# Optimization experiments

Hardware: AMD Instinct MI355X
Metric: run time of the kernel (lower is better)

Reference implementation:

```python
import jax, jax.numpy as jnp
import numpy as np

T, E, H, K, WCNT, L = 131072, 512, 512, 1024, 50000, 128
NUM_LAYERS = 1


def setup_inputs() -> dict:
    key = jax.random.key(0)
    ks = jax.random.split(key, 12)
    f32 = jnp.float32
    return {
        "topic": jax.random.randint(ks[0], (L,), 0, WCNT, dtype=jnp.int32),
        "score_s": jax.random.uniform(ks[1], (1,), dtype=f32),
        "emb": jax.random.normal(ks[2], (WCNT, E), dtype=f32) * 0.05,
        "h": jax.random.normal(ks[3], (NUM_LAYERS, 1, H), dtype=f32) * 0.05,
        "vs": jax.random.normal(ks[4], (T, E), dtype=f32) * 0.05,
        "hs": jax.random.normal(ks[5], (T, 1, H), dtype=f32) * 0.05,
        "w_ih": jax.random.normal(ks[6], (3 * H, 2 * E + 1), dtype=f32) * 0.02,
        "w_hh": jax.random.normal(ks[7], (3 * H, H), dtype=f32) * 0.02,
        "b_ih": jnp.zeros((3 * H,), f32),
        "b_hh": jnp.zeros((3 * H,), f32),
        "w_score": jax.random.normal(ks[8], (1, E + 2 * H + 1), dtype=f32) * 0.02,
        "b_score": jnp.zeros((1,), f32),
    }


def _forward(topic, score_s, emb, h, vs, hs, w_ih, w_hh, b_ih, b_hh, w_score, b_score):
    # topic embedding: mean of word vectors -> v [E]
    v = emb[topic].mean(axis=0)
    # dot-product attention over growing history
    alpha = vs @ v                               # [T]
    vals, idx = jax.lax.top_k(alpha, K)          # top-k similar past items
    a = jax.nn.softmax(vals)                     # [K]
    hs_flat = hs.reshape(-1, NUM_LAYERS * H)     # [T, H]
    attn_h = a @ hs_flat[idx]                    # [H] weighted combine of gathered states
    length = jnp.full((1,), K, dtype=v.dtype)
    # with_last=True: cat([v, attn_h, h, length])
    pred_v = jnp.concatenate([v, attn_h, h.reshape(-1), length])[None, :]  # [1, E+2H+1]
    score = pred_v @ w_score.T + b_score         # [1, 1]
    # score_mode='double': split v by correctness of s
    pos = (score_s >= 0.5).astype(v.dtype)[0]
    x = jnp.concatenate([v * pos, v * (1.0 - pos), score_s])  # [2E+1]
    # single GRU step (torch gate layout: r, z, n)
    h_prev = h.reshape(H)
    gi = w_ih @ x + b_ih
    gh = w_hh @ h_prev + b_hh
    r = jax.nn.sigmoid(gi[:H] + gh[:H])
    z = jax.nn.sigmoid(gi[H:2 * H] + gh[H:2 * H])
    n = jnp.tanh(gi[2 * H:] + r * gh[2 * H:])
    h_new = ((1.0 - z) * n + z * h_prev).reshape(NUM_LAYERS, 1, H)
    # LSTMA updates the history
    vs_new = jnp.concatenate([vs, v[None, :]], axis=0)
    hs_new = jnp.concatenate([hs, h_new], axis=0)
    return score, h_new, vs_new, hs_new


def reference(topic, score_s, emb, h, vs, hs, w_ih, w_hh, b_ih, b_hh, w_score, b_score):
    return _forward(topic, score_s, emb, h, vs, hs, w_ih, w_hh, b_ih, b_hh, w_score, b_score)
```

## Files before the change

kernel.cpp:

```cpp
#include <hip/hip_runtime.h>
#include <math.h>

constexpr int T_ = 131072;
constexpr int E_ = 512;
constexpr int H_ = 512;
constexpr int K_ = 1024;
constexpr int L_ = 128;

typedef __attribute__((ext_vector_type(4))) float f32x4;

constexpr size_t OFF_V     = 0;
constexpr size_t OFF_ALPHA = 512;
constexpr size_t OFF_HIST1 = OFF_ALPHA + T_;
constexpr size_t OFF_HIST2 = OFF_HIST1 + 65536;
constexpr size_t OFF_CNT   = OFF_HIST2 + 65536;
constexpr size_t OFF_INFO  = OFF_CNT + 2;
constexpr size_t OFF_VALS  = OFF_INFO + 8;
constexpr size_t OFF_IDX   = OFF_VALS + K_;
constexpr size_t OFF_GI    = OFF_IDX + K_;
constexpr size_t OFF_GH    = OFF_GI + 3 * H_;

constexpr int ZERO_N = 65536 + 65536 + 2;

constexpr size_t OUT_VS = 513;
constexpr size_t OUT_HS = 513 + (size_t)(T_ + 1) * E_;

__device__ __forceinline__ unsigned fkey(float f) {
    unsigned u = __float_as_uint(f);
    return (u & 0x80000000u) ? ~u : (u | 0x80000000u);
}

__global__ __launch_bounds__(1024) void k_init(const int* __restrict__ topic,
                                               const float* __restrict__ emb,
                                               float* __restrict__ ws_v,
                                               unsigned* __restrict__ zero_base,
                                               float* __restrict__ out) {
    if (blockIdx.x == gridDim.x - 1) {
        __shared__ float part[512];
        int t = threadIdx.x;
        int e = t & 511, g = t >> 9;
        float s = 0.f;
        #pragma unroll 8
        for (int l = g * 64; l < g * 64 + 64; ++l) {
            int tp = topic[l];
            s += emb[(size_t)tp * E_ + e];
        }
        if (g == 1) part[e] = s;
        __syncthreads();
        if (g == 0) {
            float v = (s + part[e]) * (1.0f / L_);
            ws_v[e] = v;
            out[OUT_VS + (size_t)T_ * E_ + e] = v;
        }
    } else {
        int i = blockIdx.x * blockDim.x + threadIdx.x;
        if (i < ZERO_N) zero_base[i] = 0u;
    }
}

__global__ __launch_bounds__(256) void k_mega(const float* __restrict__ vs,
                                              const float* __restrict__ hs,
                                              const float* __restrict__ ws_v,
                                              float* __restrict__ alpha,
                                              unsigned* __restrict__ hist1,
                                              float* __restrict__ out) {
    int wave = threadIdx.x >> 6, lane = threadIdx.x & 63;
    int b = blockIdx.x;
    bool is_vs = b < (T_ / 4);
    int row = (is_vs ? b : b - T_ / 4) * 4 + wave;
    const f32x4* src4 = (const f32x4*)((is_vs ? vs : hs) + (size_t)row * E_);
    f32x4 a0 = __builtin_nontemporal_load(&src4[lane]);
    f32x4 a1 = __builtin_nontemporal_load(&src4[lane + 64]);
    if (is_vs) {
        const f32x4* v4 = (const f32x4*)ws_v;
        f32x4 b0 = v4[lane];
        f32x4 b1 = v4[lane + 64];
        float dot = 0.f;
        dot = fmaf(a0.x, b0.x, dot); dot = fmaf(a0.y, b0.y, dot);
        dot = fmaf(a0.z, b0.z, dot); dot = fmaf(a0.w, b0.w, dot);
        dot = fmaf(a1.x, b1.x, dot); dot = fmaf(a1.y, b1.y, dot);
        dot = fmaf(a1.z, b1.z, dot); dot = fmaf(a1.w, b1.w, dot);
        #pragma unroll
        for (int m = 32; m; m >>= 1) dot += __shfl_xor(dot, m, 64);
        if (lane == 0) {
            alpha[row] = dot;
            atomicAdd(&hist1[fkey(dot) >> 16], 1u);
        }
    }
    int nl = (lane + 1) & 63;
    float n0x = __shfl(a0.x, nl, 64), n0y = __shfl(a0.y, nl, 64), n0z = __shfl(a0.z, nl, 64);
    float n1x = __shfl(a1.x, nl, 64), n1y = __shfl(a1.y, nl, 64), n1z = __shfl(a1.z, nl, 64);
    float* dst = out + (is_vs ? OUT_VS : OUT_HS) + (size_t)row * E_;
    f32x4* d4 = (f32x4*)(dst + 3);
    bool last = (lane == 63);
    f32x4 lo;
    lo.x = a0.w;
    lo.y = last ? n1x : n0x;
    lo.z = last ? n1y : n0y;
    lo.w = last ? n1z : n0z;
    __builtin_nontemporal_store(lo, &d4[lane]);
    if (!last) {
        f32x4 hi;
        hi.x = a1.w; hi.y = n1x; hi.z = n1y; hi.w = n1z;
        __builtin_nontemporal_store(hi, &d4[lane + 64]);
    }
    if (lane == 0) { dst[0] = a0.x; dst[1] = a0.y; dst[2] = a0.z; }
    if (last) dst[511] = a1.w;
}

__global__ __launch_bounds__(256) void k_scan(const unsigned* __restrict__ hist,
                                              unsigned* __restrict__ info, int pass) {
    __shared__ unsigned ps[256];
    __shared__ unsigned s_chunk, s_above;
    int t = threadIdx.x;
    unsigned Kwant = (pass == 0) ? (unsigned)K_ : ((unsigned)K_ - info[1]);
    unsigned base = 65536u - (unsigned)(t + 1) * 256u;
    unsigned s = 0;
    for (int j = 0; j < 256; ++j) s += hist[base + j];
    ps[t] = s;
    __syncthreads();
    #pragma unroll
    for (int off = 1; off < 256; off <<= 1) {
        unsigned v = (t >= off) ? ps[t - off] : 0u;
        __syncthreads();
        ps[t] += v;
        __syncthreads();
    }
    unsigned incl = ps[t], excl = incl - s;
    if (excl < Kwant && incl >= Kwant) { s_chunk = (unsigned)t; s_above = excl; }
    __syncthreads();
    unsigned c = s_chunk;
    unsigned Kw2 = Kwant - s_above;
    unsigned bin = 65535u - c * 256u - (unsigned)t;
    unsigned b = hist[bin];
    __syncthreads();
    ps[t] = b;
    __syncthreads();
    #pragma unroll
    for (int off = 1; off < 256; off <<= 1) {
        unsigned v = (t >= off) ? ps[t - off] : 0u;
        __syncthreads();
        ps[t] += v;
        __syncthreads();
    }
    unsigned inc2 = ps[t], ex2 = inc2 - b;
    if (ex2 < Kw2 && inc2 >= Kw2) {
        unsigned cnt_above = s_above + ex2;
        if (pass == 0) { info[0] = bin; info[1] = cnt_above; }
        else {
            info[2] = (info[0] << 16) | bin;
            info[3] = info[1] + cnt_above;
            info[4] = (unsigned)K_ - info[3];
        }
    }
}

__global__ __launch_bounds__(256) void k_hist2(const float* __restrict__ alpha,
                                               const unsigned* __restrict__ info,
                                               unsigned* __restrict__ hist2) {
    int i = blockIdx.x * blockDim.x + threadIdx.x;
    unsigned key = fkey(alpha[i]);
    if ((key >> 16) == info[0]) atomicAdd(&hist2[key & 0xFFFFu], 1u);
}

__global__ __launch_bounds__(256) void k_select(const float* __restrict__ alpha,
                                                const unsigned* __restrict__ info,
                                                unsigned* __restrict__ cnt,
                                                float* __restrict__ vals,
                                                int* __restrict__ idx) {
    int i = blockIdx.x * blockDim.x + threadIdx.x;
    float a = alpha[i];
    unsigned key = fkey(a);
    unsigned thr = info[2];
    if (key > thr) {
        unsigned p = atomicAdd(&cnt[0], 1u);
        vals[p] = a; idx[p] = i;
    } else if (key == thr) {
        unsigned t = atomicAdd(&cnt[1], 1u);
        if (t < info[4]) {
            unsigned p = info[3] + t;
            vals[p] = a; idx[p] = i;
        }
    }
}

__global__ __launch_bounds__(512) void k_attn(const float* __restrict__ hs,
                                              const float* __restrict__ vals,
                                              const int* __restrict__ idx,
                                              float* __restrict__ part) {
    __shared__ float red[512];
    int t = threadIdx.x, j = blockIdx.x;
    float v0 = vals[t], v1 = vals[t + 512];
    red[t] = fmaxf(v0, v1);
    __syncthreads();
    for (int s = 256; s > 0; s >>= 1) { if (t < s) red[t] = fmaxf(red[t], red[t + s]); __syncthreads(); }
    float m = red[0];
    __syncthreads();
    red[t] = expf(v0 - m) + expf(v1 - m);
    __syncthreads();
    for (int s = 256; s > 0; s >>= 1) { if (t < s) red[t] += red[t + s]; __syncthreads(); }
    float S = red[0];
    float acc = 0.f;
    #pragma unroll
    for (int k = j * 8; k < j * 8 + 8; ++k) {
        float w = expf(vals[k] - m) / S;
        acc = fmaf(w, hs[(size_t)idx[k] * E_ + t], acc);
    }
    part[(size_t)j * E_ + t] = acc;
}

__global__ __launch_bounds__(256) void k_gru(const float* __restrict__ wih,
                                             const float* __restrict__ whh,
                                             const float* __restrict__ bih,
                                             const float* __restrict__ bhh,
                                             const float* __restrict__ ws_v,
                                             const float* __restrict__ score_s,
                                             const float* __restrict__ h_in,
                                             float* __restrict__ gi,
                                             float* __restrict__ gh) {
    __shared__ float x[1025 + 512];
    int t = threadIdx.x;
    float ss = score_s[0];
    float pos = ss >= 0.5f ? 1.f : 0.f;
    for (int c = t; c < 1025; c += 256) {
        float xv;
        if (c < 512)       xv = ws_v[c] * pos;
        else if (c < 1024) xv = ws_v[c - 512] * (1.f - pos);
        else               xv = ss;
        x[c] = xv;
    }
    for (int c = t; c < 512; c += 256) x[1025 + c] = h_in[c];
    __syncthreads();
    int wave = t >> 6, lane = t & 63;
    int row = blockIdx.x * 4 + wave;
    const float* wr = wih + (size_t)row * 1025;
    float s1 = 0.f;
    for (int c = lane; c < 1025; c += 64) s1 = fmaf(wr[c], x[c], s1);
    const float* hr = whh + (size_t)row * 512;
    float s2 = 0.f;
    #pragma unroll
    for (int c = lane; c < 512; c += 64) s2 = fmaf(hr[c], x[1025 + c], s2);
    #pragma unroll
    for (int m = 32; m; m >>= 1) {
        s1 += __shfl_xor(s1, m, 64);
        s2 += __shfl_xor(s2, m, 64);
    }
    if (lane == 0) { gi[row] = s1 + bih[row]; gh[row] = s2 + bhh[row]; }
}

__global__ __launch_bounds__(512) void k_final(const float* __restrict__ gi,
                                               const float* __restrict__ gh,
                                               const float* __restrict__ h_in,
                                               const float* __restrict__ part,
                                               const float* __restrict__ ws_v,
                                               const float* __restrict__ w_score,
                                               const float* __restrict__ b_score,
                                               float* __restrict__ out) {
    __shared__ float red[512];
    int j = threadIdx.x;
    float r = 1.f / (1.f + expf(-(gi[j] + gh[j])));
    float z = 1.f / (1.f + expf(-(gi[H_ + j] + gh[H_ + j])));
    float n = tanhf(gi[2 * H_ + j] + r * gh[2 * H_ + j]);
    float hp = h_in[j];
    float hn = (1.f - z) * n + z * hp;
    out[1 + j] = hn;
    out[OUT_HS + (size_t)T_ * E_ + j] = hn;
    float attn = 0.f;
    for (int jj = 0; jj < 128; ++jj) attn += part[(size_t)jj * E_ + j];
    float d = ws_v[j] * w_score[j] + attn * w_score[512 + j] + hp * w_score[1024 + j];
    if (j == 0) d += 1024.0f * w_score[1536] + b_score[0];
    red[j] = d;
    __syncthreads();
    for (int s = 256; s > 0; s >>= 1) { if (j < s) red[j] += red[j + s]; __syncthreads(); }
    if (j == 0) out[0] = red[0];
}

extern "C" void kernel_launch(void* const* d_in, const int* in_sizes, int n_in,
                              void* d_out, int out_size, void* d_ws, size_t ws_size,
                              hipStream_t stream) {
    const int*   topic   = (const int*)d_in[0];
    const float* score_s = (const float*)d_in[1];
    const float* emb     = (const float*)d_in[2];
    const float* h_in    = (const float*)d_in[3];
    const float* vs      = (const float*)d_in[4];
    const float* hs      = (const float*)d_in[5];
    const float* w_ih    = (const float*)d_in[6];
    const float* w_hh    = (const float*)d_in[7];
    const float* b_ih    = (const float*)d_in[8];
    const float* b_hh    = (const float*)d_in[9];
    const float* w_score = (const float*)d_in[10];
    const float* b_score = (const float*)d_in[11];
    float* out = (float*)d_out;

    float*    wsf   = (float*)d_ws;
    float*    v_ws  = wsf + OFF_V;
    float*    alpha = wsf + OFF_ALPHA;
    unsigned* hist1 = (unsigned*)(wsf + OFF_HIST1);
    unsigned* hist2 = (unsigned*)(wsf + OFF_HIST2);
    unsigned* cnt   = (unsigned*)(wsf + OFF_CNT);
    unsigned* info  = (unsigned*)(wsf + OFF_INFO);
    float*    vals  = wsf + OFF_VALS;
    int*      idx   = (int*)(wsf + OFF_IDX);
    float*    part  = wsf + OFF_ALPHA;
    float*    gi    = wsf + OFF_GI;
    float*    gh    = wsf + OFF_GH;

    hipLaunchKernelGGL(k_init, dim3(130), dim3(1024), 0, stream,
                       topic, emb, v_ws, hist1, out);
    hipLaunchKernelGGL(k_mega, dim3(2 * (T_ / 4)), dim3(256), 0, stream,
                       vs, hs, v_ws, alpha, hist1, out);
    hipLaunchKernelGGL(k_scan, dim3(1), dim3(256), 0, stream, hist1, info, 0);
    hipLaunchKernelGGL(k_hist2, dim3(T_ / 256), dim3(256), 0, stream, alpha, info, hist2);
    hipLaunchKernelGGL(k_scan, dim3(1), dim3(256), 0, stream, hist2, info, 1);
    hipLaunchKernelGGL(k_select, dim3(T_ / 256), dim3(256), 0, stream, alpha, info, cnt, vals, idx);
    hipLaunchKernelGGL(k_attn, dim3(128), dim3(512), 0, stream, hs, vals, idx, part);
    hipLaunchKernelGGL(k_gru, dim3(384), dim3(256), 0, stream,
                       w_ih, w_hh, b_ih, b_hh, v_ws, score_s, h_in, gi, gh);
    hipLaunchKernelGGL(k_final, dim3(1), dim3(512), 0, stream,
                       gi, gh, h_in, part, v_ws, w_score, b_score, out);
}
```

Baseline: 244.9 us.

## Fuse top-k select, attention and GRU tail into one persistent kernel with grid barriers

Replaces seven small launches (two scans, hist2, select, attention, GRU, final) with a single 512-block kernel that uses atomic-counter grid barriers between phases, so launch gaps and per-kernel ramp-up disappear. The attention and GRU matvec now run concurrently in disjoint block ranges. Nontemporal stores in the main copy kernel are also swapped for regular stores. The grid barriers rely on all 512 blocks being co-resident and on the counters being zeroed each call; a spin barrier can add latency and will deadlock if residency fails.

```diff
diff --git a/kernel.cpp b/kernel.cpp
--- a/kernel.cpp
+++ b/kernel.cpp
@@ -6,6 +6,7 @@
 constexpr int H_ = 512;
 constexpr int K_ = 1024;
 constexpr int L_ = 128;
+constexpr unsigned NB_TAIL = 512;
 
 typedef __attribute__((ext_vector_type(4))) float f32x4;
 
@@ -14,13 +15,14 @@
 constexpr size_t OFF_HIST1 = OFF_ALPHA + T_;
 constexpr size_t OFF_HIST2 = OFF_HIST1 + 65536;
 constexpr size_t OFF_CNT   = OFF_HIST2 + 65536;
-constexpr size_t OFF_INFO  = OFF_CNT + 2;
+constexpr size_t OFF_CTR   = OFF_CNT + 2;
+constexpr size_t OFF_INFO  = OFF_CTR + 8;
 constexpr size_t OFF_VALS  = OFF_INFO + 8;
 constexpr size_t OFF_IDX   = OFF_VALS + K_;
 constexpr size_t OFF_GI    = OFF_IDX + K_;
 constexpr size_t OFF_GH    = OFF_GI + 3 * H_;
 
-constexpr int ZERO_N = 65536 + 65536 + 2;
+constexpr int ZERO_N = 65536 + 65536 + 2 + 8;
 
 constexpr size_t OUT_VS = 513;
 constexpr size_t OUT_HS = 513 + (size_t)(T_ + 1) * E_;
@@ -28,6 +30,16 @@
 __device__ __forceinline__ unsigned fkey(float f) {
     unsigned u = __float_as_uint(f);
     return (u & 0x80000000u) ? ~u : (u | 0x80000000u);
+}
+
+__device__ __forceinline__ void gbar(unsigned* c) {
+    __syncthreads();
+    if (threadIdx.x == 0) {
+        __hip_atomic_fetch_add(c, 1u, __ATOMIC_ACQ_REL, __HIP_MEMORY_SCOPE_AGENT);
+        while (__hip_atomic_load(c, __ATOMIC_ACQUIRE, __HIP_MEMORY_SCOPE_AGENT) < NB_TAIL)
+            __builtin_amdgcn_s_sleep(4);
+    }
+    __syncthreads();
 }
 
 __global__ __launch_bounds__(1024) void k_init(const int* __restrict__ topic,
@@ -98,20 +110,18 @@
     lo.y = last ? n1x : n0x;
     lo.z = last ? n1y : n0y;
     lo.w = last ? n1z : n0z;
-    __builtin_nontemporal_store(lo, &d4[lane]);
+    d4[lane] = lo;
     if (!last) {
         f32x4 hi;
         hi.x = a1.w; hi.y = n1x; hi.z = n1y; hi.w = n1z;
-        __builtin_nontemporal_store(hi, &d4[lane + 64]);
+        d4[lane + 64] = hi;
     }
     if (lane == 0) { dst[0] = a0.x; dst[1] = a0.y; dst[2] = a0.z; }
     if (last) dst[511] = a1.w;
 }
 
-__global__ __launch_bounds__(256) void k_scan(const unsigned* __restrict__ hist,
-                                              unsigned* __restrict__ info, int pass) {
-    __shared__ unsigned ps[256];
-    __shared__ unsigned s_chunk, s_above;
+__device__ void scan_body(const unsigned* __restrict__ hist,
+                          unsigned* __restrict__ info, int pass, unsigned* ps) {
     int t = threadIdx.x;
     unsigned Kwant = (pass == 0) ? (unsigned)K_ : ((unsigned)K_ - info[1]);
     unsigned base = 65536u - (unsigned)(t + 1) * 256u;
@@ -127,14 +137,14 @@
         __syncthreads();
     }
     unsigned incl = ps[t], excl = incl - s;
-    if (excl < Kwant && incl >= Kwant) { s_chunk = (unsigned)t; s_above = excl; }
-    __syncthreads();
-    unsigned c = s_chunk;
-    unsigned Kw2 = Kwant - s_above;
+    if (excl < Kwant && incl >= Kwant) { ps[256] = (unsigned)t; ps[257] = excl; }
+    __syncthreads();
+    unsigned c = ps[256], above = ps[257];
+    unsigned Kw2 = Kwant - above;
     unsigned bin = 65535u - c * 256u - (unsigned)t;
-    unsigned b = hist[bin];
-    __syncthreads();
-    ps[t] = b;
+    unsigned bv = hist[bin];
+    __syncthreads();
+    ps[t] = bv;
     __syncthreads();
     #pragma unroll
     for (int off = 1; off < 256; off <<= 1) {
@@ -143,136 +153,138 @@
         ps[t] += v;
         __syncthreads();
     }
-    unsigned inc2 = ps[t], ex2 = inc2 - b;
+    unsigned inc2 = ps[t], ex2 = inc2 - bv;
     if (ex2 < Kw2 && inc2 >= Kw2) {
-        unsigned cnt_above = s_above + ex2;
-        if (pass == 0) { info[0] = bin; info[1] = cnt_above; }
+        unsigned ca = above + ex2;
+        if (pass == 0) { info[0] = bin; info[1] = ca; }
         else {
             info[2] = (info[0] << 16) | bin;
-            info[3] = info[1] + cnt_above;
+            info[3] = info[1] + ca;
             info[4] = (unsigned)K_ - info[3];
         }
     }
 }
 
-__global__ __launch_bounds__(256) void k_hist2(const float* __restrict__ alpha,
-                                               const unsigned* __restrict__ info,
-                                               unsigned* __restrict__ hist2) {
-    int i = blockIdx.x * blockDim.x + threadIdx.x;
-    unsigned key = fkey(alpha[i]);
+__global__ __launch_bounds__(256) void k_tail(
+    const float* __restrict__ alpha_r, float* __restrict__ part,
+    unsigned* __restrict__ hist1, unsigned* __restrict__ hist2,
+    unsigned* __restrict__ cnt, unsigned* __restrict__ info,
+    unsigned* __restrict__ ctr,
+    float* __restrict__ vals, int* __restrict__ idx,
+    const float* __restrict__ hs,
+    const float* __restrict__ wih, const float* __restrict__ whh,
+    const float* __restrict__ bih, const float* __restrict__ bhh,
+    const float* __restrict__ ws_v, const float* __restrict__ score_s,
+    const float* __restrict__ h_in,
+    float* __restrict__ gi, float* __restrict__ gh,
+    const float* __restrict__ w_score, const float* __restrict__ b_score,
+    float* __restrict__ out)
+{
+    __shared__ float shf[1544];
+    unsigned* shu = (unsigned*)shf;
+    int t = threadIdx.x, b = blockIdx.x;
+    int i = b * 256 + t;
+
+    if (b == 0) scan_body(hist1, info, 0, shu);
+    gbar(&ctr[0]);
+
+    float av = alpha_r[i];
+    unsigned key = fkey(av);
     if ((key >> 16) == info[0]) atomicAdd(&hist2[key & 0xFFFFu], 1u);
-}
-
-__global__ __launch_bounds__(256) void k_select(const float* __restrict__ alpha,
-                                                const unsigned* __restrict__ info,
-                                                unsigned* __restrict__ cnt,
-                                                float* __restrict__ vals,
-                                                int* __restrict__ idx) {
-    int i = blockIdx.x * blockDim.x + threadIdx.x;
-    float a = alpha[i];
-    unsigned key = fkey(a);
-    unsigned thr = info[2];
-    if (key > thr) {
-        unsigned p = atomicAdd(&cnt[0], 1u);
-        vals[p] = a; idx[p] = i;
-    } else if (key == thr) {
-        unsigned t = atomicAdd(&cnt[1], 1u);
-        if (t < info[4]) {
-            unsigned p = info[3] + t;
-            vals[p] = a; idx[p] = i;
-        }
-    }
-}
-
-__global__ __launch_bounds__(512) void k_attn(const float* __restrict__ hs,
-                                              const float* __restrict__ vals,
-                                              const int* __restrict__ idx,
-                                              float* __restrict__ part) {
-    __shared__ float red[512];
-    int t = threadIdx.x, j = blockIdx.x;
-    float v0 = vals[t], v1 = vals[t + 512];
-    red[t] = fmaxf(v0, v1);
-    __syncthreads();
-    for (int s = 256; s > 0; s >>= 1) { if (t < s) red[t] = fmaxf(red[t], red[t + s]); __syncthreads(); }
-    float m = red[0];
-    __syncthreads();
-    red[t] = expf(v0 - m) + expf(v1 - m);
-    __syncthreads();
-    for (int s = 256; s > 0; s >>= 1) { if (t < s) red[t] += red[t + s]; __syncthreads(); }
-    float S = red[0];
-    float acc = 0.f;
-    #pragma unroll
-    for (int k = j * 8; k < j * 8 + 8; ++k) {
-        float w = expf(vals[k] - m) / S;
-        acc = fmaf(w, hs[(size_t)idx[k] * E_ + t], acc);
-    }
-    part[(size_t)j * E_ + t] = acc;
-}
-
-__global__ __launch_bounds__(256) void k_gru(const float* __restrict__ wih,
-                                             const float* __restrict__ whh,
-                                             const float* __restrict__ bih,
-                                             const float* __restrict__ bhh,
-                                             const float* __restrict__ ws_v,
-                                             const float* __restrict__ score_s,
-                                             const float* __restrict__ h_in,
-                                             float* __restrict__ gi,
-                                             float* __restrict__ gh) {
-    __shared__ float x[1025 + 512];
-    int t = threadIdx.x;
-    float ss = score_s[0];
-    float pos = ss >= 0.5f ? 1.f : 0.f;
-    for (int c = t; c < 1025; c += 256) {
-        float xv;
-        if (c < 512)       xv = ws_v[c] * pos;
-        else if (c < 1024) xv = ws_v[c - 512] * (1.f - pos);
-        else               xv = ss;
-        x[c] = xv;
-    }
-    for (int c = t; c < 512; c += 256) x[1025 + c] = h_in[c];
-    __syncthreads();
-    int wave = t >> 6, lane = t & 63;
-    int row = blockIdx.x * 4 + wave;
-    const float* wr = wih + (size_t)row * 1025;
-    float s1 = 0.f;
-    for (int c = lane; c < 1025; c += 64) s1 = fmaf(wr[c], x[c], s1);
-    const float* hr = whh + (size_t)row * 512;
-    float s2 = 0.f;
-    #pragma unroll
-    for (int c = lane; c < 512; c += 64) s2 = fmaf(hr[c], x[1025 + c], s2);
-    #pragma unroll
-    for (int m = 32; m; m >>= 1) {
-        s1 += __shfl_xor(s1, m, 64);
-        s2 += __shfl_xor(s2, m, 64);
-    }
-    if (lane == 0) { gi[row] = s1 + bih[row]; gh[row] = s2 + bhh[row]; }
-}
-
-__global__ __launch_bounds__(512) void k_final(const float* __restrict__ gi,
-                                               const float* __restrict__ gh,
-                                               const float* __restrict__ h_in,
-                                               const float* __restrict__ part,
-                                               const float* __restrict__ ws_v,
-                                               const float* __restrict__ w_score,
-                                               const float* __restrict__ b_score,
-                                               float* __restrict__ out) {
-    __shared__ float red[512];
-    int j = threadIdx.x;
-    float r = 1.f / (1.f + expf(-(gi[j] + gh[j])));
-    float z = 1.f / (1.f + expf(-(gi[H_ + j] + gh[H_ + j])));
-    float n = tanhf(gi[2 * H_ + j] + r * gh[2 * H_ + j]);
-    float hp = h_in[j];
-    float hn = (1.f - z) * n + z * hp;
-    out[1 + j] = hn;
-    out[OUT_HS + (size_t)T_ * E_ + j] = hn;
-    float attn = 0.f;
-    for (int jj = 0; jj < 128; ++jj) attn += part[(size_t)jj * E_ + j];
-    float d = ws_v[j] * w_score[j] + attn * w_score[512 + j] + hp * w_score[1024 + j];
-    if (j == 0) d += 1024.0f * w_score[1536] + b_score[0];
-    red[j] = d;
-    __syncthreads();
-    for (int s = 256; s > 0; s >>= 1) { if (j < s) red[j] += red[j + s]; __syncthreads(); }
-    if (j == 0) out[0] = red[0];
+    gbar(&ctr[1]);
+
+    if (b == 0) scan_body(hist2, info, 1, shu);
+    gbar(&ctr[2]);
+
+    {
+        unsigned thr = info[2];
+        if (key > thr) {
+            unsigned p = atomicAdd(&cnt[0], 1u);
+            vals[p] = av; idx[p] = i;
+        } else if (key == thr) {
+            unsigned tt = atomicAdd(&cnt[1], 1u);
+            if (tt < info[4]) {
+                unsigned p = info[3] + tt;
+                vals[p] = av; idx[p] = i;
+            }
+        }
+    }
+    gbar(&ctr[3]);
+
+    if (b < 128) {
+        float v0 = vals[t], v1 = vals[t + 256], v2 = vals[t + 512], v3 = vals[t + 768];
+        shf[t] = fmaxf(fmaxf(v0, v1), fmaxf(v2, v3));
+        __syncthreads();
+        for (int s = 128; s > 0; s >>= 1) { if (t < s) shf[t] = fmaxf(shf[t], shf[t + s]); __syncthreads(); }
+        float m = shf[0];
+        __syncthreads();
+        shf[t] = expf(v0 - m) + expf(v1 - m) + expf(v2 - m) + expf(v3 - m);
+        __syncthreads();
+        for (int s = 128; s > 0; s >>= 1) { if (t < s) shf[t] += shf[t + s]; __syncthreads(); }
+        float S = shf[0];
+        float acc0 = 0.f, acc1 = 0.f;
+        #pragma unroll
+        for (int k = b * 8; k < b * 8 + 8; ++k) {
+            float w = expf(vals[k] - m) / S;
+            const float* hr = hs + (size_t)idx[k] * E_;
+            acc0 = fmaf(w, hr[t], acc0);
+            acc1 = fmaf(w, hr[t + 256], acc1);
+        }
+        part[(size_t)b * E_ + t] = acc0;
+        part[(size_t)b * E_ + t + 256] = acc1;
+    } else {
+        int bb = b - 128;
+        float ss = score_s[0];
+        float pos = ss >= 0.5f ? 1.f : 0.f;
+        for (int c = t; c < 1025; c += 256) {
+            float xv;
+            if (c < 512)       xv = ws_v[c] * pos;
+            else if (c < 1024) xv = ws_v[c - 512] * (1.f - pos);
+            else               xv = ss;
+            shf[c] = xv;
+        }
+        for (int c = t; c < 512; c += 256) shf[1025 + c] = h_in[c];
+        __syncthreads();
+        int wave = t >> 6, lane = t & 63;
+        int row = bb * 4 + wave;
+        const float* wr = wih + (size_t)row * 1025;
+        float s1 = 0.f;
+        for (int c = lane; c < 1025; c += 64) s1 = fmaf(wr[c], shf[c], s1);
+        const float* hr2 = whh + (size_t)row * 512;
+        float s2 = 0.f;
+        #pragma unroll
+        for (int c = lane; c < 512; c += 64) s2 = fmaf(hr2[c], shf[1025 + c], s2);
+        #pragma unroll
+        for (int m2 = 32; m2; m2 >>= 1) {
+            s1 += __shfl_xor(s1, m2, 64);
+            s2 += __shfl_xor(s2, m2, 64);
+        }
+        if (lane == 0) { gi[row] = s1 + bih[row]; gh[row] = s2 + bhh[row]; }
+    }
+    gbar(&ctr[4]);
+
+    if (b == 0) {
+        float dsum = 0.f;
+        #pragma unroll
+        for (int half = 0; half < 2; ++half) {
+            int j = t + half * 256;
+            float r = 1.f / (1.f + expf(-(gi[j] + gh[j])));
+            float z = 1.f / (1.f + expf(-(gi[H_ + j] + gh[H_ + j])));
+            float n = tanhf(gi[2 * H_ + j] + r * gh[2 * H_ + j]);
+            float hp = h_in[j];
+            float hn = (1.f - z) * n + z * hp;
+            out[1 + j] = hn;
+            out[OUT_HS + (size_t)T_ * E_ + j] = hn;
+            float attn = 0.f;
+            for (int jj = 0; jj < 128; ++jj) attn += part[(size_t)jj * E_ + j];
+            dsum += ws_v[j] * w_score[j] + attn * w_score[512 + j] + hp * w_score[1024 + j];
+        }
+        if (t == 0) dsum += 1024.0f * w_score[1536] + b_score[0];
+        shf[t] = dsum;
+        __syncthreads();
+        for (int s = 128; s > 0; s >>= 1) { if (t < s) shf[t] += shf[t + s]; __syncthreads(); }
+        if (t == 0) out[0] = shf[0];
+    }
 }
 
 extern "C" void kernel_launch(void* const* d_in, const int* in_sizes, int n_in,
@@ -298,6 +310,7 @@
     unsigned* hist1 = (unsigned*)(wsf + OFF_HIST1);
     unsigned* hist2 = (unsigned*)(wsf + OFF_HIST2);
     unsigned* cnt   = (unsigned*)(wsf + OFF_CNT);
+    unsigned* ctr   = (unsigned*)(wsf + OFF_CTR);
     unsigned* info  = (unsigned*)(wsf + OFF_INFO);
     float*    vals  = wsf + OFF_VALS;
     int*      idx   = (int*)(wsf + OFF_IDX);
@@ -309,13 +322,8 @@
                        topic, emb, v_ws, hist1, out);
     hipLaunchKernelGGL(k_mega, dim3(2 * (T_ / 4)), dim3(256), 0, stream,
                        vs, hs, v_ws, alpha, hist1, out);
-    hipLaunchKernelGGL(k_scan, dim3(1), dim3(256), 0, stream, hist1, info, 0);
-    hipLaunchKernelGGL(k_hist2, dim3(T_ / 256), dim3(256), 0, stream, alpha, info, hist2);
-    hipLaunchKernelGGL(k_scan, dim3(1), dim3(256), 0, stream, hist2, info, 1);
-    hipLaunchKernelGGL(k_select, dim3(T_ / 256), dim3(256), 0, stream, alpha, info, cnt, vals, idx);
-    hipLaunchKernelGGL(k_attn, dim3(128), dim3(512), 0, stream, hs, vals, idx, part);
-    hipLaunchKernelGGL(k_gru, dim3(384), dim3(256), 0, stream,
-                       w_ih, w_hh, b_ih, b_hh, v_ws, score_s, h_in, gi, gh);
-    hipLaunchKernelGGL(k_final, dim3(1), dim3(512), 0, stream,
-                       gi, gh, h_in, part, v_ws, w_score, b_score, out);
-}
+    hipLaunchKernelGGL(k_tail, dim3(NB_TAIL), dim3(256), 0, stream,
+                       alpha, part, hist1, hist2, cnt, info, ctr, vals, idx,
+                       hs, w_ih, w_hh, b_ih, b_hh, v_ws, score_s, h_in,
+                       gi, gh, w_score, b_score, out);
+}
```

Result: slower. 461.4 us (+88.4%).
